# Kernel tuning notes

Measured on AMD Instinct MI355X. Metric: run time of the kernel, lower is better.

Reference implementation:

```python
import jax, jax.numpy as jnp
import numpy as np

B, CIN, T, H, W = 1, 256, 64, 32, 32
A, G = 8, 8
SCALES = jnp.array([1., 2., 4., 8., 16., 32., 64., 128.], dtype=jnp.float32)
FEAT_STRIDE = 8.0
NMS_TOP_N = 100
NMS_THRESH = 0.7
MIN_SIZE = 4.0
POS_THR, NEG_THR = 0.7, 0.3
NEG_INF = -1e9


def _conv3d(x, w, b, strides):
    y = jax.lax.conv_general_dilated(
        x, w, window_strides=strides, padding=[(1, 1)] * 3,
        dimension_numbers=('NCDHW', 'OIDHW', 'NCDHW'))
    return y + b[None, :, None, None, None]


def _iou(a, b):
    # 1D interval IoU; a, b broadcastable [..., 2] = (start, end)
    inter = jnp.maximum(jnp.minimum(a[..., 1], b[..., 1]) - jnp.maximum(a[..., 0], b[..., 0]), 0.0)
    union = (a[..., 1] - a[..., 0]) + (b[..., 1] - b[..., 0]) - inter
    return inter / jnp.maximum(union, 1e-6)


def _nms(boxes, scores):
    # greedy 1D NMS: boxes [N,2], scores [N] -> top NMS_TOP_N (zero-padded)
    n = scores.shape[0]
    def step(sc, _):
        i = jnp.argmax(sc)
        s, box = sc[i], boxes[i]
        sup = (_iou(box[None], boxes) > NMS_THRESH) | (jnp.arange(n) == i)
        return jnp.where(sup, NEG_INF, sc), (box, s)
    _, (kb, ks) = jax.lax.scan(step, scores, None, length=NMS_TOP_N)
    keep = ks > NEG_INF * 0.5
    return jnp.where(keep[:, None], kb, 0.0), jnp.where(keep, ks, 0.0)


def _forward(base_feat, gt_chunks, video_len, c1w, c1b, c2w, c2b, sw, sb, dw, db):
    bsz = base_feat.shape[0]
    x = _conv3d(base_feat, c1w, c1b, (1, 2, 2))
    x = _conv3d(x, c2w, c2b, (1, 2, 2))
    feat = jnp.max(x, axis=(3, 4))                       # AdaptiveMaxPool3d((None,1,1)) -> [B,512,T]
    tlen = feat.shape[2]
    score_logit = (jnp.einsum('oc,bct->bot', sw, feat) + sb[None, :, None]).reshape(bsz, 2, A, tlen)
    delta = (jnp.einsum('oc,bct->bot', dw, feat) + db[None, :, None]).reshape(bsz, 2, A, tlen)
    prob = jax.nn.softmax(score_logit, axis=1)
    logp = jax.nn.log_softmax(score_logit, axis=1)

    # anchors: A lengths x T temporal positions, flattened as a*T + t
    anchor_len = FEAT_STRIDE * SCALES                                    # [A]
    centers = (jnp.arange(tlen, dtype=jnp.float32) + 0.5) * FEAT_STRIDE  # [T]
    a_start = centers[None, :] - anchor_len[:, None] / 2                 # [A,T]
    a_end = centers[None, :] + anchor_len[:, None] / 2
    anchors = jnp.stack([a_start, a_end], -1).reshape(-1, 2)             # [N,2]
    N = A * tlen

    # ---- proposal decode + NMS ----
    dc, dl = delta[:, 0], delta[:, 1]                                    # [B,A,T]
    pc = centers[None, None, :] + dc * anchor_len[None, :, None]
    pl = anchor_len[None, :, None] * jnp.exp(jnp.clip(dl, -10.0, 10.0))
    lim = tlen * FEAT_STRIDE
    ps = jnp.clip(pc - pl / 2, 0.0, lim)
    pe = jnp.clip(pc + pl / 2, 0.0, lim)
    boxes = jnp.stack([ps, pe], -1).reshape(bsz, N, 2)
    fg = prob[:, 1].reshape(bsz, N)
    fg = jnp.where((pe - ps).reshape(bsz, N) >= MIN_SIZE, fg, NEG_INF)
    prop_coord, prop_score = jax.vmap(_nms)(boxes, fg)

    # ---- IoU-based label assignment ----
    ious = _iou(anchors[None, :, None, :], gt_chunks[:, None, :, :])     # [B,N,G]
    max_iou = ious.max(-1)
    arg = ious.argmax(-1)                                                # [B,N]
    label = jnp.where(max_iou < NEG_THR, 0, -1)
    label = jnp.where(max_iou >= POS_THR, 1, label)
    best = ious.argmax(1)                                                # best anchor per gt [B,G]
    bidx = jnp.arange(bsz)[:, None]
    label = label.at[bidx, best].set(1)
    vl = video_len.astype(jnp.float32)[:, None]
    inside = (anchors[None, :, 0] >= 0.0) & (anchors[None, :, 1] <= vl)
    label = jnp.where(inside, label, -1)

    matched = gt_chunks[bidx, arg]                                       # [B,N,2]
    gc = (matched[..., 0] + matched[..., 1]) / 2
    gl = jnp.maximum(matched[..., 1] - matched[..., 0], 1e-6)
    ac = (anchors[:, 0] + anchors[:, 1]) / 2
    al = anchors[:, 1] - anchors[:, 0]
    reg_label = jnp.stack([(gc - ac[None]) / al[None], jnp.log(gl / al[None])], -1)
    reg_label = jax.lax.stop_gradient(reg_label)                          # targets carry no grad

    # ---- losses ----
    logp2 = logp.reshape(bsz, 2, N).transpose(0, 2, 1)                   # [B,N,2]
    lab = jnp.maximum(label, 0)
    nll = -jnp.take_along_axis(logp2, lab[..., None], axis=2)[..., 0]
    mask = (label >= 0).astype(jnp.float32)
    cls_loss = (nll * mask).sum() / jnp.maximum(mask.sum(), 1.0)

    delta2 = delta.reshape(bsz, 2, N).transpose(0, 2, 1)                 # [B,N,2]
    d = delta2 - reg_label
    sl1 = jnp.where(jnp.abs(d) < 1.0, 0.5 * d * d, jnp.abs(d) - 0.5).sum(-1)
    pos = (label == 1).astype(jnp.float32)
    reg_loss = (sl1 * pos).sum() / jnp.maximum(pos.sum(), 1.0)
    return prop_coord, prop_score, cls_loss, reg_loss


def setup_inputs() -> dict:
    key = jax.random.key(0)
    ks = jax.random.split(key, 8)
    base_feat = jax.random.normal(ks[0], (B, CIN, T, H, W), jnp.float32)
    starts = jax.random.uniform(ks[1], (B, G), minval=0.0, maxval=448.0)
    lens = jax.random.uniform(ks[2], (B, G), minval=8.0, maxval=64.0)
    gt_chunks = jnp.stack([starts, jnp.clip(starts + lens, 0.0, T * FEAT_STRIDE)], -1)
    video_len = jnp.full((B,), int(T * FEAT_STRIDE), jnp.int32)
    s = 0.02
    return dict(
        base_feat=base_feat, gt_chunks=gt_chunks, video_len=video_len,
        conv1_w=jax.random.normal(ks[3], (512, CIN, 3, 3, 3), jnp.float32) * s,
        conv1_b=jnp.zeros((512,), jnp.float32),
        conv2_w=jax.random.normal(ks[4], (512, 512, 3, 3, 3), jnp.float32) * s,
        conv2_b=jnp.zeros((512,), jnp.float32),
        score_w=jax.random.normal(ks[5], (2 * A, 512), jnp.float32) * s,
        score_b=jnp.zeros((2 * A,), jnp.float32),
        delta_w=jax.random.normal(ks[6], (2 * A, 512), jnp.float32) * s,
        delta_b=jnp.zeros((2 * A,), jnp.float32),
    )


def reference(base_feat, gt_chunks, video_len, conv1_w, conv1_b, conv2_w, conv2_b, score_w, score_b, delta_w, delta_b):
    return _forward(base_feat, gt_chunks, video_len, conv1_w, conv1_b, conv2_w, conv2_b, score_w, score_b, delta_w, delta_b)
```

## Files before the change

kernel.cpp:

```cpp
#include <hip/hip_runtime.h>

typedef __attribute__((ext_vector_type(8))) _Float16 half8;
typedef __attribute__((ext_vector_type(4))) _Float16 half4;
typedef __attribute__((ext_vector_type(4))) float floatx4;

#define DI __device__ __forceinline__

DI void gl_lds16(const void* g, void* l) {
    __builtin_amdgcn_global_load_lds(
        (__attribute__((address_space(1))) void*)(g),
        (__attribute__((address_space(3))) void*)(l), 16, 0, 0);
}


__global__ __launch_bounds__(256) void wt_split_t(
        const float* __restrict__ w1, _Float16* __restrict__ w1I,
        const float* __restrict__ w2, _Float16* __restrict__ w2I,
        float* __restrict__ zp) {
    __shared__ float L[13824];
    const int b = blockIdx.x;
    const int tid = threadIdx.x;
    if (b == 0 && tid < 64) zp[tid] = 0.0f;
    if (b < 512) {
        const float* src = w1 + (size_t)b * 6912;
        for (int idx = tid; idx < 6912; idx += 256) L[idx] = src[idx] * 64.0f;
        __syncthreads();
        for (int c = tid; c < 864; c += 256) {
            const int tap = c >> 5, o = c & 31;
            half8 h, l;
#pragma unroll
            for (int j = 0; j < 8; ++j) {
                const float x = L[(o * 8 + j) * 27 + tap];
                const _Float16 hh = (_Float16)x;
                h[j] = hh; l[j] = (_Float16)(x - (float)hh);
            }
            const size_t off = (size_t)b * 13824 + (size_t)(tap * 8 + (o >> 2)) * 64 + (o & 3) * 8;
            *(half8*)&w1I[off] = h;
            *(half8*)&w1I[off + 32] = l;
        }
    } else {
        const float* src = w2 + (size_t)(b - 512) * 13824;
        for (int idx = tid; idx < 13824; idx += 256) L[idx] = src[idx] * 64.0f;
        __syncthreads();
        for (int c = tid; c < 1728; c += 256) {
            const int tap = c >> 6, o = c & 63;
            half8 h, l;
#pragma unroll
            for (int j = 0; j < 8; ++j) {
                const float x = L[(o * 8 + j) * 27 + tap];
                const _Float16 hh = (_Float16)x;
                h[j] = hh; l[j] = (_Float16)(x - (float)hh);
            }
            const size_t off = (size_t)(b - 512) * 27648 + (size_t)(tap * 16 + (o >> 2)) * 64 + (o & 3) * 8;
            *(half8*)&w2I[off] = h;
            *(half8*)&w2I[off + 32] = l;
        }
    }
}

__global__ __launch_bounds__(256) void in_split(const float* __restrict__ in,
                                                _Float16* __restrict__ oI) {
    __shared__ float T[128 * 65];
    const int hb = blockIdx.x;
    const int s0 = blockIdx.y * 64;
    const int tid = threadIdx.x;
    const int cil = tid >> 1, part = tid & 1;
    const float* src = in + (size_t)(hb * 128 + cil) * 65536 + s0 + part * 32;
    float v[32];
#pragma unroll
    for (int q = 0; q < 8; ++q) *(float4*)(v + q * 4) = *(const float4*)(src + q * 4);
#pragma unroll
    for (int j = 0; j < 32; ++j) T[cil * 65 + part * 32 + j] = v[j];
    __syncthreads();
#pragma unroll
    for (int k = 0; k < 4; ++k) {
        const int c = tid + k * 256;
        const int sp = c >> 4, ol = c & 15;
        half8 h, l;
#pragma unroll
        for (int j = 0; j < 8; ++j) {
            const float x = T[(ol * 8 + j) * 65 + sp];
            const _Float16 hh = (_Float16)x;
            h[j] = hh; l[j] = (_Float16)(x - (float)hh);
        }
        const int og = hb * 16 + ol;
        const size_t off = (size_t)(s0 + sp) * 512 + (size_t)(og >> 2) * 64 + (og & 3) * 8;
        *(half8*)&oI[off] = h;
        *(half8*)&oI[off + 32] = l;
    }
}

__global__ __launch_bounds__(256, 2) void conv1_mfma(
        const _Float16* __restrict__ xI, const _Float16* __restrict__ wI,
        const float* __restrict__ b1, const _Float16* __restrict__ zp,
        _Float16* __restrict__ yI) {
    __shared__ __align__(16) _Float16 A2[2][128 * 64];
    __shared__ __align__(16) _Float16 B3[3][128 * 64];
    const int tid = threadIdx.x;
    const int n_ = blockIdx.x;
    const int t = ((n_ & 7) << 3) | ((n_ >> 3) & 7);
    const int co_blk = (n_ >> 6) & 3;
    const int h0 = ((n_ >> 8) & 1) * 8;
    const int wid = tid >> 6, lane = tid & 63;
    const int wm = wid & 1, wn = wid >> 1;
    const int ml = lane & 15, ql = lane >> 4;
    const int cs0 = (ql ^ (ml & 7)) * 8;
    const int cs1 = ((4 + ql) ^ (ml & 7)) * 8;
    const int sl = lane & 7, rl = lane >> 3;
    const int lc = sl ^ rl;

    const _Float16* wA[4]; const _Float16* bB[4];
    int dstq[4]; bool hok[4], wok[4];
    const size_t wbo = (size_t)co_blk * 128 * 13824;
#pragma unroll
    for (int q = 0; q < 4; ++q) {
        const int row = (q * 4 + wid) * 8 + rl;
        wA[q] = wI + wbo + (size_t)row * 13824 + lc * 8;
        dstq[q] = (q * 4 + wid) * 512 + lane * 8;
        const int h = h0 + (row >> 4), w = row & 15;
        const int ih2 = 2 * h - 1, iw2 = 2 * w - 1;
        hok[q] = (ih2 >= 0); wok[q] = (iw2 >= 0);
        bB[q] = xI + (ptrdiff_t)(ih2 * 32 + iw2) * 512 + lc * 8;
    }
    const _Float16* zpl = zp + lc * 8;

    floatx4 zz = {0.f, 0.f, 0.f, 0.f};
    floatx4 acc[4][4];
#pragma unroll
    for (int i = 0; i < 4; ++i)
#pragma unroll
        for (int j = 0; j < 4; ++j) acc[i][j] = zz;

    auto stageA = [&](int kt, int cb, int KH, int KW, _Float16* Ad) {
        const size_t ab = (size_t)(((kt * 9 + KH * 3 + KW) * 8 + cb) * 64);
#pragma unroll
        for (int q = 0; q < 4; ++q) gl_lds16(wA[q] + ab, &Ad[dstq[q]]);
    };
    auto stageB = [&](int kt, int cb, int KH, int KW, _Float16* Bd) {
        const int it = t + kt - 1;
        const bool tok = ((unsigned)it < 64u);
        const ptrdiff_t boff = (ptrdiff_t)it * 524288 + KH * 16384 + KW * 512 + cb * 64;
#pragma unroll
        for (int q = 0; q < 4; ++q) {
            const bool ok = tok && (KH > 0 || hok[q]) && (KW > 0 || wok[q]);
            gl_lds16(ok ? (bB[q] + boff) : zpl, &Bd[dstq[q]]);
        }
    };

    stageA(0, 0, 0, 0, A2[0]);
    stageB(0, 0, 0, 0, B3[0]);
    stageB(0, 0, 0, 1, B3[1]);
    asm volatile("s_waitcnt vmcnt(4)" ::: "memory");
    __builtin_amdgcn_s_barrier();

    for (int o = 0; o < 24; ++o) {
        const int cb = o / 3, kt = o - cb * 3;
        const int o1 = o + 1;
        const int cb1 = o1 / 3, kt1 = o1 - cb1 * 3;
#pragma unroll
        for (int j = 0; j < 9; ++j) {
            const int par = (o + j) & 1;
            if (j < 8) stageA(kt, cb, (j + 1) / 3, (j + 1) % 3, A2[par ^ 1]);
            else       stageA(kt1, cb1, 0, 0, A2[par ^ 1]);
            if (j < 7)       stageB(kt, cb, (j + 2) / 3, (j + 2) % 3, B3[(j + 2) % 3]);
            else if (j == 7) stageB(kt1, cb1, 0, 0, B3[0]);
            else             stageB(kt1, cb1, 0, 1, B3[1]);

            const _Float16* Ab = A2[par];
            const _Float16* Bb = B3[j % 3];
            half8 ah[4], alo[4], bh8[4], blo[4];
#pragma unroll
            for (int mi = 0; mi < 4; ++mi) {
                ah[mi]  = *(const half8*)&Ab[(wm * 64 + mi * 16 + ml) * 64 + cs0];
                alo[mi] = *(const half8*)&Ab[(wm * 64 + mi * 16 + ml) * 64 + cs1];
            }
#pragma unroll
            for (int ni = 0; ni < 4; ++ni) {
                bh8[ni] = *(const half8*)&Bb[(wn * 64 + ni * 16 + ml) * 64 + cs0];
                blo[ni] = *(const half8*)&Bb[(wn * 64 + ni * 16 + ml) * 64 + cs1];
            }
            __builtin_amdgcn_s_setprio(1);
#pragma unroll
            for (int mi = 0; mi < 4; ++mi)
#pragma unroll
                for (int ni = 0; ni < 4; ++ni) {
                    acc[mi][ni] = __builtin_amdgcn_mfma_f32_16x16x32_f16(ah[mi],  bh8[ni], acc[mi][ni], 0, 0, 0);
                    acc[mi][ni] = __builtin_amdgcn_mfma_f32_16x16x32_f16(ah[mi],  blo[ni], acc[mi][ni], 0, 0, 0);
                    acc[mi][ni] = __builtin_amdgcn_mfma_f32_16x16x32_f16(alo[mi], bh8[ni], acc[mi][ni], 0, 0, 0);
                }
            __builtin_amdgcn_s_setprio(0);
            asm volatile("s_waitcnt vmcnt(4)" ::: "memory");
            __builtin_amdgcn_s_barrier();
        }
    }

    const int qr = ql * 4;
#pragma unroll
    for (int mi = 0; mi < 4; ++mi) {
        const int co = co_blk * 128 + wm * 64 + mi * 16 + qr;
#pragma unroll
        for (int ni = 0; ni < 4; ++ni) {
            const int n = wn * 64 + ni * 16 + ml;
            const int h = h0 + (n >> 4), w = n & 15;
            const size_t base = ((size_t)t * 256 + h * 16 + w) * 1024
                              + (size_t)(co >> 5) * 64 + (co & 31);
            half4 hv, lv;
#pragma unroll
            for (int r = 0; r < 4; ++r) {
                const float v = acc[mi][ni][r] * 0.015625f + b1[co + r];
                const _Float16 hb = (_Float16)v;
                hv[r] = hb;
                lv[r] = (_Float16)(v - (float)hb);
            }
            *(half4*)(yI + base) = hv;
            *(half4*)(yI + base + 32) = lv;
        }
    }
}

__global__ __launch_bounds__(256, 2) void conv2_mfma(
        const _Float16* __restrict__ xI, const _Float16* __restrict__ wI,
        const _Float16* __restrict__ zp,
        float* __restrict__ x2p) {
    __shared__ __align__(16) _Float16 A2[2][128 * 64];
    __shared__ __align__(16) _Float16 B3[3][128 * 64];
    const int tid = threadIdx.x;
    const int n_ = blockIdx.x;
    const int tp = ((n_ & 7) << 2) | ((n_ >> 3) & 3);
    const int co_blk = (n_ >> 5) & 3;
    const int ks = (n_ >> 7) & 3;
    const int wid = tid >> 6, lane = tid & 63;
    const int wm = wid & 1, wn = wid >> 1;
    const int ml = lane & 15, ql = lane >> 4;
    const int cs0 = (ql ^ (ml & 7)) * 8;
    const int cs1 = ((4 + ql) ^ (ml & 7)) * 8;
    const int sl = lane & 7, rl = lane >> 3;
    const int lc = sl ^ rl;

    const _Float16* wA[4]; const _Float16* bB[4];
    int dstq[4], itv[4]; bool hok[4], wok[4];
    const size_t wbo = (size_t)co_blk * 128 * 27648;
#pragma unroll
    for (int q = 0; q < 4; ++q) {
        const int row = (q * 4 + wid) * 8 + rl;
        wA[q] = wI + wbo + (size_t)row * 27648 + lc * 8;
        dstq[q] = (q * 4 + wid) * 512 + lane * 8;
        const int sp = row & 63;
        itv[q] = tp * 2 + (row >> 6) - 1;
        const int ih2 = 2 * (sp >> 3) - 1, iw2 = 2 * (sp & 7) - 1;
        hok[q] = (ih2 >= 0); wok[q] = (iw2 >= 0);
        bB[q] = xI + (ptrdiff_t)((itv[q] * 256 + ih2 * 16 + iw2) * 1024) + lc * 8;
    }
    const _Float16* zpl = zp + lc * 8;

    floatx4 zz = {0.f, 0.f, 0.f, 0.f};
    floatx4 acc[4][4];
#pragma unroll
    for (int i = 0; i < 4; ++i)
#pragma unroll
        for (int j = 0; j < 4; ++j) acc[i][j] = zz;

    auto stageA = [&](int kt, int cb, int KH, int KW, _Float16* Ad) {
        const size_t ab = (size_t)(((kt * 9 + KH * 3 + KW) * 16 + cb) * 64);
#pragma unroll
        for (int q = 0; q < 4; ++q) gl_lds16(wA[q] + ab, &Ad[dstq[q]]);
    };
    auto stageB = [&](int kt, int cb, int KH, int KW, _Float16* Bd) {
        const ptrdiff_t boff = (ptrdiff_t)kt * 262144 + KH * 16384 + KW * 1024 + cb * 64;
#pragma unroll
        for (int q = 0; q < 4; ++q) {
            const bool ok = ((unsigned)(itv[q] + kt) < 64u)
                         && (KH > 0 || hok[q]) && (KW > 0 || wok[q]);
            gl_lds16(ok ? (bB[q] + boff) : zpl, &Bd[dstq[q]]);
        }
    };

    stageA(0, ks * 4, 0, 0, A2[0]);
    stageB(0, ks * 4, 0, 0, B3[0]);
    stageB(0, ks * 4, 0, 1, B3[1]);
    asm volatile("s_waitcnt vmcnt(4)" ::: "memory");
    __builtin_amdgcn_s_barrier();

    for (int o = 0; o < 12; ++o) {
        const int kt = o % 3, cb = ks * 4 + o / 3;
        const int o1 = o + 1;
        const int kt1 = o1 % 3, cb1 = ks * 4 + o1 / 3;
#pragma unroll
        for (int j = 0; j < 9; ++j) {
            const int par = (o + j) & 1;
            if (j < 8) stageA(kt, cb, (j + 1) / 3, (j + 1) % 3, A2[par ^ 1]);
            else       stageA(kt1, cb1, 0, 0, A2[par ^ 1]);
            if (j < 7)       stageB(kt, cb, (j + 2) / 3, (j + 2) % 3, B3[(j + 2) % 3]);
            else if (j == 7) stageB(kt1, cb1, 0, 0, B3[0]);
            else             stageB(kt1, cb1, 0, 1, B3[1]);

            const _Float16* Ab = A2[par];
            const _Float16* Bb = B3[j % 3];
            half8 ah[4], alo[4], bh8[4], blo[4];
#pragma unroll
            for (int mi = 0; mi < 4; ++mi) {
                ah[mi]  = *(const half8*)&Ab[(wm * 64 + mi * 16 + ml) * 64 + cs0];
                alo[mi] = *(const half8*)&Ab[(wm * 64 + mi * 16 + ml) * 64 + cs1];
            }
#pragma unroll
            for (int ni = 0; ni < 4; ++ni) {
                bh8[ni] = *(const half8*)&Bb[(wn * 64 + ni * 16 + ml) * 64 + cs0];
                blo[ni] = *(const half8*)&Bb[(wn * 64 + ni * 16 + ml) * 64 + cs1];
            }
            __builtin_amdgcn_s_setprio(1);
#pragma unroll
            for (int mi = 0; mi < 4; ++mi)
#pragma unroll
                for (int ni = 0; ni < 4; ++ni) {
                    acc[mi][ni] = __builtin_amdgcn_mfma_f32_16x16x32_f16(ah[mi],  bh8[ni], acc[mi][ni], 0, 0, 0);
                    acc[mi][ni] = __builtin_amdgcn_mfma_f32_16x16x32_f16(ah[mi],  blo[ni], acc[mi][ni], 0, 0, 0);
                    acc[mi][ni] = __builtin_amdgcn_mfma_f32_16x16x32_f16(alo[mi], bh8[ni], acc[mi][ni], 0, 0, 0);
                }
            __builtin_amdgcn_s_setprio(0);
            asm volatile("s_waitcnt vmcnt(4)" ::: "memory");
            __builtin_amdgcn_s_barrier();
        }
    }

    const int qr = ql * 4;
#pragma unroll
    for (int mi = 0; mi < 4; ++mi) {
        const int co = co_blk * 128 + wm * 64 + mi * 16 + qr;
#pragma unroll
        for (int ni = 0; ni < 4; ++ni) {
            const int n = wn * 64 + ni * 16 + ml;
            const int ng = tp * 128 + n;
            float4 v;
            v.x = acc[mi][ni][0]; v.y = acc[mi][ni][1];
            v.z = acc[mi][ni][2]; v.w = acc[mi][ni][3];
            *(float4*)&x2p[((size_t)ks * 4096 + ng) * 512 + co] = v;
        }
    }
}

__global__ __launch_bounds__(256) void feat_head(
        const float* __restrict__ x2p, const float* __restrict__ b2,
        const float* __restrict__ sw, const float* __restrict__ sb,
        const float* __restrict__ dw, const float* __restrict__ db,
        float* __restrict__ scoreL, float* __restrict__ deltaL) {
    __shared__ float fr[512];
    __shared__ float partial[32][8];
    const int t = blockIdx.x, tid = threadIdx.x;
#pragma unroll
    for (int cc = 0; cc < 2; ++cc) {
        const int c = tid + cc * 256;
        float mx = -3.4e38f;
        for (int sp = 0; sp < 64; ++sp) {
            const size_t ng = (size_t)t * 64 + sp;
            const float s = x2p[ng * 512 + c]
                          + x2p[((size_t)4096 + ng) * 512 + c]
                          + x2p[((size_t)8192 + ng) * 512 + c]
                          + x2p[((size_t)12288 + ng) * 512 + c];
            mx = fmaxf(mx, s);
        }
        fr[c] = mx * 0.015625f + b2[c];
    }
    __syncthreads();
    const int o = tid & 31, part = tid >> 5;
    const float* wrow = (o < 16) ? (sw + (size_t)o * 512) : (dw + (size_t)(o - 16) * 512);
    float s = 0.f;
    const int j0 = part * 64;
#pragma unroll 16
    for (int j = 0; j < 64; ++j) s += wrow[j0 + j] * fr[j0 + j];
    partial[o][part] = s;
    __syncthreads();
    if (tid < 32) {
        float tot = 0.f;
#pragma unroll
        for (int p = 0; p < 8; ++p) tot += partial[tid][p];
        tot += (tid < 16) ? sb[tid] : db[tid - 16];
        if (tid < 16) scoreL[tid * 64 + t] = tot;
        else deltaL[(tid - 16) * 64 + t] = tot;
    }
}

__global__ void nms_loss_kernel(const float* __restrict__ scoreL,
                                const float* __restrict__ deltaL,
                                const float* __restrict__ gt,
                                const int* __restrict__ video_len,
                                float* __restrict__ out) {
    const int lane = threadIdx.x & 63;
    float gsv[8], gev[8];
#pragma unroll
    for (int g = 0; g < 8; ++g) { gsv[g] = gt[2 * g]; gev[g] = gt[2 * g + 1]; }
    const float center = ((float)lane + 0.5f) * 8.0f;
    float psv[8], pev[8], fg[8], l0v[8], l1v[8], dcv[8], dlv[8];
#pragma unroll
    for (int j = 0; j < 8; ++j) {
        const float s0 = scoreL[j * 64 + lane], s1 = scoreL[(8 + j) * 64 + lane];
        const float mm = fmaxf(s0, s1);
        const float lse = mm + logf(expf(s0 - mm) + expf(s1 - mm));
        l0v[j] = s0 - lse; l1v[j] = s1 - lse;
        const float dc = deltaL[j * 64 + lane], dl = deltaL[(8 + j) * 64 + lane];
        dcv[j] = dc; dlv[j] = dl;
        const float alen = 8.0f * (float)(1 << j);
        const float pc = center + dc * alen;
        const float pl = alen * expf(fminf(fmaxf(dl, -10.0f), 10.0f));
        const float ps = fminf(fmaxf(pc - pl * 0.5f, 0.0f), 512.0f);
        const float pe = fminf(fmaxf(pc + pl * 0.5f, 0.0f), 512.0f);
        psv[j] = ps; pev[j] = pe;
        fg[j] = ((pe - ps) >= 4.0f) ? expf(l1v[j]) : -1e9f;
    }
    for (int itn = 0; itn < 100; ++itn) {
        float v = fg[0]; int idx = lane;
#pragma unroll
        for (int j = 1; j < 8; ++j) if (fg[j] > v) { v = fg[j]; idx = lane + 64 * j; }
#pragma unroll
        for (int off = 32; off > 0; off >>= 1) {
            const float ov = __shfl_down(v, off);
            const int oi = __shfl_down(idx, off);
            if (ov > v || (ov == v && oi < idx)) { v = ov; idx = oi; }
        }
        v = __shfl(v, 0); idx = __shfl(idx, 0);
        const int wj = idx >> 6, wl = idx & 63;
        float bw0 = 0.f, bw1 = 0.f;
#pragma unroll
        for (int j = 0; j < 8; ++j) if (j == wj) { bw0 = psv[j]; bw1 = pev[j]; }
        const float b0 = __shfl(bw0, wl);
        const float b1 = __shfl(bw1, wl);
        if (lane == 0) {
            const bool kept = v > -5e8f;
            out[2 * itn] = kept ? b0 : 0.0f;
            out[2 * itn + 1] = kept ? b1 : 0.0f;
            out[200 + itn] = kept ? v : 0.0f;
        }
#pragma unroll
        for (int j = 0; j < 8; ++j) {
            const int n = lane + 64 * j;
            const float inter = fmaxf(fminf(b1, pev[j]) - fmaxf(b0, psv[j]), 0.0f);
            const float uni = (b1 - b0) + (pev[j] - psv[j]) - inter;
            const float iou = inter / fmaxf(uni, 1e-6f);
            if (iou > 0.7f || n == idx) fg[j] = -1e9f;
        }
    }
    int labv[8], aggv[8];
#pragma unroll
    for (int j = 0; j < 8; ++j) {
        const float alen = 8.0f * (float)(1 << j);
        const float as_ = center - alen * 0.5f, ae_ = center + alen * 0.5f;
        float mx = -1.0f; int ag = 0;
#pragma unroll
        for (int g = 0; g < 8; ++g) {
            const float inter = fmaxf(fminf(ae_, gev[g]) - fmaxf(as_, gsv[g]), 0.0f);
            const float uni = (ae_ - as_) + (gev[g] - gsv[g]) - inter;
            const float iou = inter / fmaxf(uni, 1e-6f);
            if (iou > mx) { mx = iou; ag = g; }
        }
        labv[j] = (mx < 0.3f) ? 0 : ((mx >= 0.7f) ? 1 : -1);
        aggv[j] = ag;
    }
    for (int g = 0; g < 8; ++g) {
        float v = -1.0f; int idx = 0;
#pragma unroll
        for (int j = 0; j < 8; ++j) {
            const int n = lane + 64 * j;
            const float alen = 8.0f * (float)(1 << j);
            const float as_ = center - alen * 0.5f, ae_ = center + alen * 0.5f;
            const float inter = fmaxf(fminf(ae_, gev[g]) - fmaxf(as_, gsv[g]), 0.0f);
            const float uni = (ae_ - as_) + (gev[g] - gsv[g]) - inter;
            const float iou = inter / fmaxf(uni, 1e-6f);
            if (iou > v || (iou == v && n < idx)) { v = iou; idx = n; }
        }
#pragma unroll
        for (int off = 32; off > 0; off >>= 1) {
            const float ov = __shfl_down(v, off);
            const int oi = __shfl_down(idx, off);
            if (ov > v || (ov == v && oi < idx)) { v = ov; idx = oi; }
        }
        idx = __shfl(idx, 0);
#pragma unroll
        for (int j = 0; j < 8; ++j)
            if (lane == (idx & 63) && j == (idx >> 6)) labv[j] = 1;
    }
    const float vl = (float)video_len[0];
    float nll_s = 0.f, msk_s = 0.f, reg_s = 0.f, pos_s = 0.f;
#pragma unroll
    for (int j = 0; j < 8; ++j) {
        const float alen = 8.0f * (float)(1 << j);
        const float as_ = center - alen * 0.5f, ae_ = center + alen * 0.5f;
        int l = labv[j];
        if (!((as_ >= 0.0f) && (ae_ <= vl))) l = -1;
        if (l >= 0) {
            msk_s += 1.0f;
            nll_s -= (l == 1) ? l1v[j] : l0v[j];
            if (l == 1) {
                pos_s += 1.0f;
                float gcv = 0.f, glv = 0.f;
#pragma unroll
                for (int g = 0; g < 8; ++g)
                    if (g == aggv[j]) {
                        gcv = (gsv[g] + gev[g]) * 0.5f;
                        glv = fmaxf(gev[g] - gsv[g], 1e-6f);
                    }
                const float r0 = (gcv - center) / alen;
                const float r1 = logf(glv / alen);
                const float d0 = dcv[j] - r0, d1 = dlv[j] - r1;
                float s = (fabsf(d0) < 1.0f) ? (0.5f * d0 * d0) : (fabsf(d0) - 0.5f);
                s += (fabsf(d1) < 1.0f) ? (0.5f * d1 * d1) : (fabsf(d1) - 0.5f);
                reg_s += s;
            }
        }
    }
    float sums[4] = {nll_s, msk_s, reg_s, pos_s};
#pragma unroll
    for (int k = 0; k < 4; ++k)
#pragma unroll
        for (int off = 32; off > 0; off >>= 1) sums[k] += __shfl_down(sums[k], off);
    if (lane == 0) {
        out[300] = sums[0] / fmaxf(sums[1], 1.0f);
        out[301] = sums[2] / fmaxf(sums[3], 1.0f);
    }
}

extern "C" void kernel_launch(void* const* d_in, const int* in_sizes, int n_in,
                              void* d_out, int out_size, void* d_ws, size_t ws_size,
                              hipStream_t stream) {
    const float* base_feat = (const float*)d_in[0];
    const float* gt        = (const float*)d_in[1];
    const int*   video_len = (const int*)d_in[2];
    const float* w1        = (const float*)d_in[3];
    const float* b1        = (const float*)d_in[4];
    const float* w2        = (const float*)d_in[5];
    const float* b2        = (const float*)d_in[6];
    const float* sw        = (const float*)d_in[7];
    const float* sb        = (const float*)d_in[8];
    const float* dw        = (const float*)d_in[9];
    const float* db        = (const float*)d_in[10];

    char* ws = (char*)d_ws;
    _Float16* w1I = (_Float16*)ws;  ws += (size_t)512 * 13824 * 2;
    _Float16* w2I = (_Float16*)ws;  ws += (size_t)512 * 27648 * 2;
    _Float16* inI = (_Float16*)ws;  ws += (size_t)65536 * 512 * 2;
    _Float16* x1I = (_Float16*)ws;  ws += (size_t)16384 * 1024 * 2;
    float* scoreL = (float*)ws;     ws += (size_t)16 * 64 * 4;
    float* deltaL = (float*)ws;     ws += (size_t)16 * 64 * 4;
    float* zpage  = (float*)ws;     ws += (size_t)64 * 4;
    float* x2p = (float*)inI;

    wt_split_t<<<1024, 256, 0, stream>>>(w1, w1I, w2, w2I, zpage);
    in_split<<<dim3(2, 1024), 256, 0, stream>>>(base_feat, inI);
    conv1_mfma<<<512, 256, 0, stream>>>(inI, w1I, b1,
                                        (const _Float16*)zpage, x1I);
    conv2_mfma<<<512, 256, 0, stream>>>(x1I, w2I,
                                        (const _Float16*)zpage, x2p);
    feat_head<<<64, 256, 0, stream>>>(x2p, b2, sw, sb, dw, db, scoreL, deltaL);
    nms_loss_kernel<<<1, 64, 0, stream>>>(scoreL, deltaL, gt, video_len,
                                          (float*)d_out);
}
```

Before: 731.0 us.

## Double the N tile of both conv kernels to 256 with 512-thread blocks

Both conv MFMA kernels now launch 512-thread blocks of eight waves covering a 128x256 output tile instead of 128x128, and the grid is halved to 256 blocks. Each weight (A) tile staged in LDS is now shared by twice as many output columns, which cuts weight reloads from global memory. In exchange the B buffers double in size, raising LDS use per block to about 128 KB, which may limit residency to one block per CU. Only 256 blocks are launched, which may leave some CUs idle or underfilled.

```diff
diff --git a/kernel.cpp b/kernel.cpp
--- a/kernel.cpp
+++ b/kernel.cpp
@@ -90,17 +90,16 @@
     }
 }
 
-__global__ __launch_bounds__(256, 2) void conv1_mfma(
+__global__ __launch_bounds__(512, 2) void conv1_mfma(
         const _Float16* __restrict__ xI, const _Float16* __restrict__ wI,
         const float* __restrict__ b1, const _Float16* __restrict__ zp,
         _Float16* __restrict__ yI) {
     __shared__ __align__(16) _Float16 A2[2][128 * 64];
-    __shared__ __align__(16) _Float16 B3[3][128 * 64];
+    __shared__ __align__(16) _Float16 B3[3][256 * 64];
     const int tid = threadIdx.x;
     const int n_ = blockIdx.x;
     const int t = ((n_ & 7) << 3) | ((n_ >> 3) & 7);
     const int co_blk = (n_ >> 6) & 3;
-    const int h0 = ((n_ >> 8) & 1) * 8;
     const int wid = tid >> 6, lane = tid & 63;
     const int wm = wid & 1, wn = wid >> 1;
     const int ml = lane & 15, ql = lane >> 4;
@@ -109,15 +108,20 @@
     const int sl = lane & 7, rl = lane >> 3;
     const int lc = sl ^ rl;
 
-    const _Float16* wA[4]; const _Float16* bB[4];
-    int dstq[4]; bool hok[4], wok[4];
+    const _Float16* wA[2]; int dstA[2];
+    const _Float16* bB[4]; int dstB[4]; bool hok[4], wok[4];
     const size_t wbo = (size_t)co_blk * 128 * 13824;
 #pragma unroll
+    for (int q = 0; q < 2; ++q) {
+        const int row = (q * 8 + wid) * 8 + rl;
+        wA[q] = wI + wbo + (size_t)row * 13824 + lc * 8;
+        dstA[q] = (q * 8 + wid) * 512 + lane * 8;
+    }
+#pragma unroll
     for (int q = 0; q < 4; ++q) {
-        const int row = (q * 4 + wid) * 8 + rl;
-        wA[q] = wI + wbo + (size_t)row * 13824 + lc * 8;
-        dstq[q] = (q * 4 + wid) * 512 + lane * 8;
-        const int h = h0 + (row >> 4), w = row & 15;
+        const int row = (q * 8 + wid) * 8 + rl;
+        dstB[q] = (q * 8 + wid) * 512 + lane * 8;
+        const int h = row >> 4, w = row & 15;
         const int ih2 = 2 * h - 1, iw2 = 2 * w - 1;
         hok[q] = (ih2 >= 0); wok[q] = (iw2 >= 0);
         bB[q] = xI + (ptrdiff_t)(ih2 * 32 + iw2) * 512 + lc * 8;
@@ -134,7 +138,7 @@
     auto stageA = [&](int kt, int cb, int KH, int KW, _Float16* Ad) {
         const size_t ab = (size_t)(((kt * 9 + KH * 3 + KW) * 8 + cb) * 64);
 #pragma unroll
-        for (int q = 0; q < 4; ++q) gl_lds16(wA[q] + ab, &Ad[dstq[q]]);
+        for (int q = 0; q < 2; ++q) gl_lds16(wA[q] + ab, &Ad[dstA[q]]);
     };
     auto stageB = [&](int kt, int cb, int KH, int KW, _Float16* Bd) {
         const int it = t + kt - 1;
@@ -143,7 +147,7 @@
 #pragma unroll
         for (int q = 0; q < 4; ++q) {
             const bool ok = tok && (KH > 0 || hok[q]) && (KW > 0 || wok[q]);
-            gl_lds16(ok ? (bB[q] + boff) : zpl, &Bd[dstq[q]]);
+            gl_lds16(ok ? (bB[q] + boff) : zpl, &Bd[dstB[q]]);
         }
     };
 
@@ -201,8 +205,7 @@
 #pragma unroll
         for (int ni = 0; ni < 4; ++ni) {
             const int n = wn * 64 + ni * 16 + ml;
-            const int h = h0 + (n >> 4), w = n & 15;
-            const size_t base = ((size_t)t * 256 + h * 16 + w) * 1024
+            const size_t base = ((size_t)t * 256 + n) * 1024
                               + (size_t)(co >> 5) * 64 + (co & 31);
             half4 hv, lv;
 #pragma unroll
@@ -218,17 +221,17 @@
     }
 }
 
-__global__ __launch_bounds__(256, 2) void conv2_mfma(
+__global__ __launch_bounds__(512, 2) void conv2_mfma(
         const _Float16* __restrict__ xI, const _Float16* __restrict__ wI,
         const _Float16* __restrict__ zp,
         float* __restrict__ x2p) {
     __shared__ __align__(16) _Float16 A2[2][128 * 64];
-    __shared__ __align__(16) _Float16 B3[3][128 * 64];
+    __shared__ __align__(16) _Float16 B3[3][256 * 64];
     const int tid = threadIdx.x;
     const int n_ = blockIdx.x;
-    const int tp = ((n_ & 7) << 2) | ((n_ >> 3) & 3);
-    const int co_blk = (n_ >> 5) & 3;
-    const int ks = (n_ >> 7) & 3;
+    const int tp = ((n_ & 7) << 1) | ((n_ >> 3) & 1);
+    const int co_blk = (n_ >> 4) & 3;
+    const int ks = (n_ >> 6) & 3;
     const int wid = tid >> 6, lane = tid & 63;
     const int wm = wid & 1, wn = wid >> 1;
     const int ml = lane & 15, ql = lane >> 4;
@@ -237,16 +240,21 @@
     const int sl = lane & 7, rl = lane >> 3;
     const int lc = sl ^ rl;
 
-    const _Float16* wA[4]; const _Float16* bB[4];
-    int dstq[4], itv[4]; bool hok[4], wok[4];
+    const _Float16* wA[2]; int dstA[2];
+    const _Float16* bB[4]; int dstB[4], itv[4]; bool hok[4], wok[4];
     const size_t wbo = (size_t)co_blk * 128 * 27648;
 #pragma unroll
+    for (int q = 0; q < 2; ++q) {
+        const int row = (q * 8 + wid) * 8 + rl;
+        wA[q] = wI + wbo + (size_t)row * 27648 + lc * 8;
+        dstA[q] = (q * 8 + wid) * 512 + lane * 8;
+    }
+#pragma unroll
     for (int q = 0; q < 4; ++q) {
-        const int row = (q * 4 + wid) * 8 + rl;
-        wA[q] = wI + wbo + (size_t)row * 27648 + lc * 8;
-        dstq[q] = (q * 4 + wid) * 512 + lane * 8;
+        const int row = (q * 8 + wid) * 8 + rl;
+        dstB[q] = (q * 8 + wid) * 512 + lane * 8;
         const int sp = row & 63;
-        itv[q] = tp * 2 + (row >> 6) - 1;
+        itv[q] = tp * 4 + (row >> 6) - 1;
         const int ih2 = 2 * (sp >> 3) - 1, iw2 = 2 * (sp & 7) - 1;
         hok[q] = (ih2 >= 0); wok[q] = (iw2 >= 0);
         bB[q] = xI + (ptrdiff_t)((itv[q] * 256 + ih2 * 16 + iw2) * 1024) + lc * 8;
@@ -263,7 +271,7 @@
     auto stageA = [&](int kt, int cb, int KH, int KW, _Float16* Ad) {
         const size_t ab = (size_t)(((kt * 9 + KH * 3 + KW) * 16 + cb) * 64);
 #pragma unroll
-        for (int q = 0; q < 4; ++q) gl_lds16(wA[q] + ab, &Ad[dstq[q]]);
+        for (int q = 0; q < 2; ++q) gl_lds16(wA[q] + ab, &Ad[dstA[q]]);
     };
     auto stageB = [&](int kt, int cb, int KH, int KW, _Float16* Bd) {
         const ptrdiff_t boff = (ptrdiff_t)kt * 262144 + KH * 16384 + KW * 1024 + cb * 64;
@@ -271,7 +279,7 @@
         for (int q = 0; q < 4; ++q) {
             const bool ok = ((unsigned)(itv[q] + kt) < 64u)
                          && (KH > 0 || hok[q]) && (KW > 0 || wok[q]);
-            gl_lds16(ok ? (bB[q] + boff) : zpl, &Bd[dstq[q]]);
+            gl_lds16(ok ? (bB[q] + boff) : zpl, &Bd[dstB[q]]);
         }
     };
 
@@ -329,7 +337,7 @@
 #pragma unroll
         for (int ni = 0; ni < 4; ++ni) {
             const int n = wn * 64 + ni * 16 + ml;
-            const int ng = tp * 128 + n;
+            const size_t ng = (size_t)tp * 256 + n;
             float4 v;
             v.x = acc[mi][ni][0]; v.y = acc[mi][ni][1];
             v.z = acc[mi][ni][2]; v.w = acc[mi][ni][3];
@@ -544,9 +552,9 @@
 
     wt_split_t<<<1024, 256, 0, stream>>>(w1, w1I, w2, w2I, zpage);
     in_split<<<dim3(2, 1024), 256, 0, stream>>>(base_feat, inI);
-    conv1_mfma<<<512, 256, 0, stream>>>(inI, w1I, b1,
+    conv1_mfma<<<256, 512, 0, stream>>>(inI, w1I, b1,
                                         (const _Float16*)zpage, x1I);
-    conv2_mfma<<<512, 256, 0, stream>>>(x1I, w2I,
+    conv2_mfma<<<256, 512, 0, stream>>>(x1I, w2I,
                                         (const _Float16*)zpage, x2p);
     feat_head<<<64, 256, 0, stream>>>(x2p, b2, sw, sb, dw, db, scoreL, deltaL);
     nms_loss_kernel<<<1, 64, 0, stream>>>(scoreL, deltaL, gt, video_len,
```

After: 789.5 us. 8.0% more time.

## Retile conv1 to 64x256 tiles with weights held in registers, fuse prep kernels

Applied to the files above, without the earlier changes.

Conv1 changes from 128 output channels by 128 spatial positions per block to 64 channels by 256 positions (a whole 16x16 plane). The weight fragments are now loaded straight into registers and double-buffered there, while only the input tile is staged in LDS, with two buffers and a full vmcnt(0) wait every step. The separate weight-split and input-split kernels are merged into one launch of 3072 blocks to save a kernel launch. This trades LDS traffic for higher register pressure and exposes global-load latency on the weight path, and the stricter wait could leave less overlap.

```diff
diff --git a/kernel.cpp b/kernel.cpp
--- a/kernel.cpp
+++ b/kernel.cpp
@@ -13,9 +13,10 @@
 }
 
 
-__global__ __launch_bounds__(256) void wt_split_t(
+__global__ __launch_bounds__(256) void prep_split(
         const float* __restrict__ w1, _Float16* __restrict__ w1I,
         const float* __restrict__ w2, _Float16* __restrict__ w2I,
+        const float* __restrict__ in, _Float16* __restrict__ oI,
         float* __restrict__ zp) {
     __shared__ float L[13824];
     const int b = blockIdx.x;
@@ -38,7 +39,7 @@
             *(half8*)&w1I[off] = h;
             *(half8*)&w1I[off + 32] = l;
         }
-    } else {
+    } else if (b < 1024) {
         const float* src = w2 + (size_t)(b - 512) * 13824;
         for (int idx = tid; idx < 13824; idx += 256) L[idx] = src[idx] * 64.0f;
         __syncthreads();
@@ -55,38 +56,34 @@
             *(half8*)&w2I[off] = h;
             *(half8*)&w2I[off + 32] = l;
         }
-    }
-}
-
-__global__ __launch_bounds__(256) void in_split(const float* __restrict__ in,
-                                                _Float16* __restrict__ oI) {
-    __shared__ float T[128 * 65];
-    const int hb = blockIdx.x;
-    const int s0 = blockIdx.y * 64;
-    const int tid = threadIdx.x;
-    const int cil = tid >> 1, part = tid & 1;
-    const float* src = in + (size_t)(hb * 128 + cil) * 65536 + s0 + part * 32;
-    float v[32];
-#pragma unroll
-    for (int q = 0; q < 8; ++q) *(float4*)(v + q * 4) = *(const float4*)(src + q * 4);
-#pragma unroll
-    for (int j = 0; j < 32; ++j) T[cil * 65 + part * 32 + j] = v[j];
-    __syncthreads();
-#pragma unroll
-    for (int k = 0; k < 4; ++k) {
-        const int c = tid + k * 256;
-        const int sp = c >> 4, ol = c & 15;
-        half8 h, l;
-#pragma unroll
-        for (int j = 0; j < 8; ++j) {
-            const float x = T[(ol * 8 + j) * 65 + sp];
-            const _Float16 hh = (_Float16)x;
-            h[j] = hh; l[j] = (_Float16)(x - (float)hh);
-        }
-        const int og = hb * 16 + ol;
-        const size_t off = (size_t)(s0 + sp) * 512 + (size_t)(og >> 2) * 64 + (og & 3) * 8;
-        *(half8*)&oI[off] = h;
-        *(half8*)&oI[off + 32] = l;
+    } else {
+        const int idx = b - 1024;
+        const int hb = idx & 1;
+        const int s0 = (idx >> 1) * 64;
+        const int cil = tid >> 1, part = tid & 1;
+        const float* src = in + (size_t)(hb * 128 + cil) * 65536 + s0 + part * 32;
+        float v[32];
+#pragma unroll
+        for (int q = 0; q < 8; ++q) *(float4*)(v + q * 4) = *(const float4*)(src + q * 4);
+#pragma unroll
+        for (int j = 0; j < 32; ++j) L[cil * 65 + part * 32 + j] = v[j];
+        __syncthreads();
+#pragma unroll
+        for (int k = 0; k < 4; ++k) {
+            const int c = tid + k * 256;
+            const int sp = c >> 4, ol = c & 15;
+            half8 h, l;
+#pragma unroll
+            for (int j = 0; j < 8; ++j) {
+                const float x = L[(ol * 8 + j) * 65 + sp];
+                const _Float16 hh = (_Float16)x;
+                h[j] = hh; l[j] = (_Float16)(x - (float)hh);
+            }
+            const int og = hb * 16 + ol;
+            const size_t off = (size_t)(s0 + sp) * 512 + (size_t)(og >> 2) * 64 + (og & 3) * 8;
+            *(half8*)&oI[off] = h;
+            *(half8*)&oI[off + 32] = l;
+        }
     }
 }
 
@@ -94,30 +91,32 @@
         const _Float16* __restrict__ xI, const _Float16* __restrict__ wI,
         const float* __restrict__ b1, const _Float16* __restrict__ zp,
         _Float16* __restrict__ yI) {
-    __shared__ __align__(16) _Float16 A2[2][128 * 64];
-    __shared__ __align__(16) _Float16 B3[3][128 * 64];
+    __shared__ __align__(16) _Float16 B2[2][256 * 64];
     const int tid = threadIdx.x;
     const int n_ = blockIdx.x;
     const int t = ((n_ & 7) << 3) | ((n_ >> 3) & 7);
-    const int co_blk = (n_ >> 6) & 3;
-    const int h0 = ((n_ >> 8) & 1) * 8;
+    const int co_blk = (n_ >> 6) & 7;
     const int wid = tid >> 6, lane = tid & 63;
-    const int wm = wid & 1, wn = wid >> 1;
     const int ml = lane & 15, ql = lane >> 4;
     const int cs0 = (ql ^ (ml & 7)) * 8;
     const int cs1 = ((4 + ql) ^ (ml & 7)) * 8;
     const int sl = lane & 7, rl = lane >> 3;
     const int lc = sl ^ rl;
 
-    const _Float16* wA[4]; const _Float16* bB[4];
-    int dstq[4]; bool hok[4], wok[4];
-    const size_t wbo = (size_t)co_blk * 128 * 13824;
-#pragma unroll
-    for (int q = 0; q < 4; ++q) {
-        const int row = (q * 4 + wid) * 8 + rl;
-        wA[q] = wI + wbo + (size_t)row * 13824 + lc * 8;
-        dstq[q] = (q * 4 + wid) * 512 + lane * 8;
-        const int h = h0 + (row >> 4), w = row & 15;
+    const _Float16* wAh[4]; const _Float16* wAl[4];
+    const size_t wbo = (size_t)co_blk * 64 * 13824;
+#pragma unroll
+    for (int mi = 0; mi < 4; ++mi) {
+        const _Float16* base = wI + wbo + (size_t)(mi * 16 + ml) * 13824 + ql * 8;
+        wAh[mi] = base; wAl[mi] = base + 32;
+    }
+    const _Float16* bB[8]; int dstB[8]; bool hok[8], wok[8];
+#pragma unroll
+    for (int q = 0; q < 8; ++q) {
+        const int rowg = q * 4 + wid;
+        const int row = rowg * 8 + rl;
+        dstB[q] = rowg * 512 + lane * 8;
+        const int h = row >> 4, w = row & 15;
         const int ih2 = 2 * h - 1, iw2 = 2 * w - 1;
         hok[q] = (ih2 >= 0); wok[q] = (iw2 >= 0);
         bB[q] = xI + (ptrdiff_t)(ih2 * 32 + iw2) * 512 + lc * 8;
@@ -131,78 +130,72 @@
 #pragma unroll
         for (int j = 0; j < 4; ++j) acc[i][j] = zz;
 
-    auto stageA = [&](int kt, int cb, int KH, int KW, _Float16* Ad) {
-        const size_t ab = (size_t)(((kt * 9 + KH * 3 + KW) * 8 + cb) * 64);
-#pragma unroll
-        for (int q = 0; q < 4; ++q) gl_lds16(wA[q] + ab, &Ad[dstq[q]]);
+    struct ARegs { half8 h[4], l[4]; };
+    ARegs aX, aY;
+    int skt = 0, skh = 0, skw = 0, scb = 0;
+
+    auto loadA = [&](int tap, int cb, ARegs& dst) {
+        const size_t aoff = (size_t)(tap * 8 + cb) * 64;
+#pragma unroll
+        for (int mi = 0; mi < 4; ++mi) {
+            dst.h[mi] = *(const half8*)(wAh[mi] + aoff);
+            dst.l[mi] = *(const half8*)(wAl[mi] + aoff);
+        }
     };
-    auto stageB = [&](int kt, int cb, int KH, int KW, _Float16* Bd) {
+    auto stageB = [&](int kt, int kh, int kw, int cb, _Float16* Bd) {
         const int it = t + kt - 1;
         const bool tok = ((unsigned)it < 64u);
-        const ptrdiff_t boff = (ptrdiff_t)it * 524288 + KH * 16384 + KW * 512 + cb * 64;
-#pragma unroll
-        for (int q = 0; q < 4; ++q) {
-            const bool ok = tok && (KH > 0 || hok[q]) && (KW > 0 || wok[q]);
-            gl_lds16(ok ? (bB[q] + boff) : zpl, &Bd[dstq[q]]);
+        const ptrdiff_t boff = (ptrdiff_t)it * 524288 + kh * 16384 + kw * 512 + cb * 64;
+#pragma unroll
+        for (int q = 0; q < 8; ++q) {
+            const bool ok = tok && (kh > 0 || hok[q]) && (kw > 0 || wok[q]);
+            gl_lds16(ok ? (bB[q] + boff) : zpl, &Bd[dstB[q]]);
         }
     };
 
-    stageA(0, 0, 0, 0, A2[0]);
-    stageB(0, 0, 0, 0, B3[0]);
-    stageB(0, 0, 0, 1, B3[1]);
-    asm volatile("s_waitcnt vmcnt(4)" ::: "memory");
+    loadA(0, 0, aX);
+    stageB(0, 0, 0, 0, B2[0]);
+    asm volatile("s_waitcnt vmcnt(0)" ::: "memory");
     __builtin_amdgcn_s_barrier();
 
-    for (int o = 0; o < 24; ++o) {
-        const int cb = o / 3, kt = o - cb * 3;
-        const int o1 = o + 1;
-        const int cb1 = o1 / 3, kt1 = o1 - cb1 * 3;
-#pragma unroll
-        for (int j = 0; j < 9; ++j) {
-            const int par = (o + j) & 1;
-            if (j < 8) stageA(kt, cb, (j + 1) / 3, (j + 1) % 3, A2[par ^ 1]);
-            else       stageA(kt1, cb1, 0, 0, A2[par ^ 1]);
-            if (j < 7)       stageB(kt, cb, (j + 2) / 3, (j + 2) % 3, B3[(j + 2) % 3]);
-            else if (j == 7) stageB(kt1, cb1, 0, 0, B3[0]);
-            else             stageB(kt1, cb1, 0, 1, B3[1]);
-
-            const _Float16* Ab = A2[par];
-            const _Float16* Bb = B3[j % 3];
-            half8 ah[4], alo[4], bh8[4], blo[4];
-#pragma unroll
-            for (int mi = 0; mi < 4; ++mi) {
-                ah[mi]  = *(const half8*)&Ab[(wm * 64 + mi * 16 + ml) * 64 + cs0];
-                alo[mi] = *(const half8*)&Ab[(wm * 64 + mi * 16 + ml) * 64 + cs1];
-            }
+    auto phase = [&](ARegs& cur, ARegs& nxt, int par) {
+        if (++skw == 3) { skw = 0; if (++skh == 3) { skh = 0; if (++skt == 3) { skt = 0; if (++scb == 8) scb = 0; } } }
+        loadA((skt * 3 + skh) * 3 + skw, scb, nxt);
+        stageB(skt, skh, skw, scb, B2[par ^ 1]);
+        const _Float16* Bb = B2[par];
+        half8 bh8[4], blo[4];
+#pragma unroll
+        for (int ni = 0; ni < 4; ++ni) {
+            bh8[ni] = *(const half8*)&Bb[(wid * 64 + ni * 16 + ml) * 64 + cs0];
+            blo[ni] = *(const half8*)&Bb[(wid * 64 + ni * 16 + ml) * 64 + cs1];
+        }
+        __builtin_amdgcn_s_setprio(1);
+#pragma unroll
+        for (int mi = 0; mi < 4; ++mi)
 #pragma unroll
             for (int ni = 0; ni < 4; ++ni) {
-                bh8[ni] = *(const half8*)&Bb[(wn * 64 + ni * 16 + ml) * 64 + cs0];
-                blo[ni] = *(const half8*)&Bb[(wn * 64 + ni * 16 + ml) * 64 + cs1];
-            }
-            __builtin_amdgcn_s_setprio(1);
-#pragma unroll
-            for (int mi = 0; mi < 4; ++mi)
-#pragma unroll
-                for (int ni = 0; ni < 4; ++ni) {
-                    acc[mi][ni] = __builtin_amdgcn_mfma_f32_16x16x32_f16(ah[mi],  bh8[ni], acc[mi][ni], 0, 0, 0);
-                    acc[mi][ni] = __builtin_amdgcn_mfma_f32_16x16x32_f16(ah[mi],  blo[ni], acc[mi][ni], 0, 0, 0);
-                    acc[mi][ni] = __builtin_amdgcn_mfma_f32_16x16x32_f16(alo[mi], bh8[ni], acc[mi][ni], 0, 0, 0);
-                }
-            __builtin_amdgcn_s_setprio(0);
-            asm volatile("s_waitcnt vmcnt(4)" ::: "memory");
-            __builtin_amdgcn_s_barrier();
-        }
+                acc[mi][ni] = __builtin_amdgcn_mfma_f32_16x16x32_f16(cur.h[mi], bh8[ni], acc[mi][ni], 0, 0, 0);
+                acc[mi][ni] = __builtin_amdgcn_mfma_f32_16x16x32_f16(cur.h[mi], blo[ni], acc[mi][ni], 0, 0, 0);
+                acc[mi][ni] = __builtin_amdgcn_mfma_f32_16x16x32_f16(cur.l[mi], bh8[ni], acc[mi][ni], 0, 0, 0);
+            }
+        __builtin_amdgcn_s_setprio(0);
+        asm volatile("s_waitcnt vmcnt(0)" ::: "memory");
+        __builtin_amdgcn_s_barrier();
+    };
+
+    for (int p = 0; p < 216; p += 2) {
+        phase(aX, aY, 0);
+        phase(aY, aX, 1);
     }
 
     const int qr = ql * 4;
 #pragma unroll
     for (int mi = 0; mi < 4; ++mi) {
-        const int co = co_blk * 128 + wm * 64 + mi * 16 + qr;
+        const int co = co_blk * 64 + mi * 16 + qr;
 #pragma unroll
         for (int ni = 0; ni < 4; ++ni) {
-            const int n = wn * 64 + ni * 16 + ml;
-            const int h = h0 + (n >> 4), w = n & 15;
-            const size_t base = ((size_t)t * 256 + h * 16 + w) * 1024
+            const int n = wid * 64 + ni * 16 + ml;
+            const size_t base = ((size_t)t * 256 + n) * 1024
                               + (size_t)(co >> 5) * 64 + (co & 31);
             half4 hv, lv;
 #pragma unroll
@@ -542,8 +535,7 @@
     float* zpage  = (float*)ws;     ws += (size_t)64 * 4;
     float* x2p = (float*)inI;
 
-    wt_split_t<<<1024, 256, 0, stream>>>(w1, w1I, w2, w2I, zpage);
-    in_split<<<dim3(2, 1024), 256, 0, stream>>>(base_feat, inI);
+    prep_split<<<3072, 256, 0, stream>>>(w1, w1I, w2, w2I, base_feat, inI, zpage);
     conv1_mfma<<<512, 256, 0, stream>>>(inI, w1I, b1,
                                         (const _Float16*)zpage, x1I);
     conv2_mfma<<<512, 256, 0, stream>>>(x1I, w2I,
```

Result: slower. 970.7 us (+32.8%).
